# Performance work log

Hardware: AMD Instinct MI355X
Metric: run time of the kernel (lower is better)

The kernel has to match this reference:

```python
import jax, jax.numpy as jnp
import numpy as np

REG = 0.01  # cfg['mf']['reg']
NUM_USERS, NUM_ITEMS, H = 100000, 1000000, 64
B, K = 16384, 50


def setup_inputs() -> dict:
    key = jax.random.key(0)
    k1, k2, k3, k4, k5 = jax.random.split(key, 5)
    return {
        "user_weight": jax.random.normal(k1, (NUM_USERS, H), dtype=jnp.float32),
        "item_weight": jax.random.normal(k2, (NUM_ITEMS, H), dtype=jnp.float32),
        "user_bias": jnp.zeros((NUM_USERS, 1), dtype=jnp.float32),
        "item_bias": jnp.zeros((NUM_ITEMS, 1), dtype=jnp.float32),
        "bias": jnp.zeros((1,), dtype=jnp.float32),
        "target": jax.random.uniform(k3, (B, K), dtype=jnp.float32),
        "user": jax.random.randint(k4, (B,), 0, NUM_USERS),
        "item": jax.random.randint(k5, (B, K), 0, NUM_ITEMS),
    }


def reference(user_weight, item_weight, user_bias, item_bias, bias, target, user, item):
    # user_embedding(u) = user_weight[u] + user_bias[u] (scalar bias broadcast over H)
    ue = user_weight[user] + user_bias[user]            # [B, H]
    ie = item_weight[item] + item_bias[item]            # [B, K, H]
    # per-user dot against its K items + global scalar bias (replaces Python loop)
    pred = jnp.einsum('bh,bkh->bk', ue, ie) + bias[0]   # [B, K]
    mse = jnp.mean((pred - target) ** 2)
    reg = REG * jnp.mean(jnp.linalg.norm(ue, axis=-1)) \
        + REG * jnp.mean(jnp.linalg.norm(ie.reshape(-1, ie.shape[-1]), axis=-1))
    loss = mse + reg
    # pack predictions and scalar loss into one array
    return jnp.concatenate([pred.ravel(), loss[None]])
```

## Files before the change

kernel.cpp:

```cpp
#include <hip/hip_runtime.h>

constexpr int NB = 16384;
constexpr int NK = 50;
constexpr int NH = 64;
constexpr float REG = 0.01f;
constexpr int G  = 4;


__global__ __launch_bounds__(256) void mf_main(
    const float* __restrict__ user_weight,
    const float* __restrict__ item_weight,
    const float* __restrict__ user_bias,
    const float* __restrict__ item_bias,
    const float* __restrict__ gbias,
    const float* __restrict__ target,
    const int*   __restrict__ user,
    const int*   __restrict__ item,
    float* __restrict__ out,
    float* __restrict__ acc)
{
    const int tid  = threadIdx.x;
    const int wave = tid >> 6;
    const int lane = tid & 63;
    const int kcl  = (lane < NK) ? lane : (NK - 1);
    const bool active = (lane < NK);

    __shared__ __align__(16) float s_ue[4][NH];
    __shared__ float s_red[3][4];

    const float gb = gbias[0];

    int b  = (blockIdx.x * 4 + wave) * G;
    int u  = user[b];
    int it = item[b * NK + kcl];

    float mse_acc = 0.f, ien_acc = 0.f, uen_acc = 0.f;

    #pragma unroll
    for (int g = 0; g < G; ++g) {
        const float ubv = user_bias[u];
        const float ibv = item_bias[it];
        const float tgt = target[b * NK + kcl];
        const float uev = user_weight[(size_t)u * NH + lane] + ubv;

        const float4* rowp = reinterpret_cast<const float4*>(item_weight + (size_t)it * NH);
        float4 r[16];
        #pragma unroll
        for (int i = 0; i < 16; ++i) r[i] = rowp[i];

        int nu = u, nit = it;
        if (g + 1 < G) {
            nu  = user[b + 1];
            nit = item[(b + 1) * NK + kcl];
        }

        s_ue[wave][lane] = uev;
        float us = uev * uev;
        #pragma unroll
        for (int off = 32; off > 0; off >>= 1) us += __shfl_down(us, off);
        if (lane == 0) uen_acc += sqrtf(us);

        const float4* uep = reinterpret_cast<const float4*>(&s_ue[wave][0]);
        float dot = 0.f, sq = 0.f;
        #pragma unroll
        for (int i = 0; i < 16; ++i) {
            const float4 ue4 = uep[i];
            const float iex = r[i].x + ibv;
            const float iey = r[i].y + ibv;
            const float iez = r[i].z + ibv;
            const float iew = r[i].w + ibv;
            dot += iex * ue4.x + iey * ue4.y + iez * ue4.z + iew * ue4.w;
            sq  += iex * iex   + iey * iey   + iez * iez   + iew * iew;
        }
        const float pred = dot + gb;
        if (active) {
            out[b * NK + lane] = pred;
            const float d = pred - tgt;
            mse_acc += d * d;
            ien_acc += sqrtf(sq);
        }

        b += 1; u = nu; it = nit;
    }

    #pragma unroll
    for (int off = 32; off > 0; off >>= 1) {
        mse_acc += __shfl_down(mse_acc, off);
        ien_acc += __shfl_down(ien_acc, off);
    }
    if (lane == 0) {
        s_red[0][wave] = mse_acc;
        s_red[1][wave] = uen_acc;
        s_red[2][wave] = ien_acc;
    }
    __syncthreads();
    if (tid == 0) {
        atomicAdd(&acc[0], s_red[0][0] + s_red[0][1] + s_red[0][2] + s_red[0][3]);
        atomicAdd(&acc[1], s_red[1][0] + s_red[1][1] + s_red[1][2] + s_red[1][3]);
        atomicAdd(&acc[2], s_red[2][0] + s_red[2][1] + s_red[2][2] + s_red[2][3]);
    }
}

__global__ void mf_finish(const float* __restrict__ acc, float* __restrict__ out)
{
    const float inv_bk = 1.0f / (float)(NB * NK);
    const float mse = acc[0] * inv_bk;
    const float loss = mse + REG * (acc[1] / (float)NB) + REG * (acc[2] * inv_bk);
    out[NB * NK] = loss;
}

extern "C" void kernel_launch(void* const* d_in, const int* in_sizes, int n_in,
                              void* d_out, int out_size, void* d_ws, size_t ws_size,
                              hipStream_t stream) {
    const float* user_weight = (const float*)d_in[0];
    const float* item_weight = (const float*)d_in[1];
    const float* user_bias   = (const float*)d_in[2];
    const float* item_bias   = (const float*)d_in[3];
    const float* gbias       = (const float*)d_in[4];
    const float* target      = (const float*)d_in[5];
    const int*   user        = (const int*)d_in[6];
    const int*   item        = (const int*)d_in[7];
    float* out = (float*)d_out;
    float* acc = (float*)d_ws;

    hipMemsetAsync(acc, 0, 3 * sizeof(float), stream);
    mf_main<<<NB / (4 * G), 256, 0, stream>>>(user_weight, item_weight, user_bias, item_bias,
                                              gbias, target, user, item, out, acc);
    mf_finish<<<1, 1, 0, stream>>>(acc, out);
}
```

Baseline: 370.4 us.

## Gather item rows cooperatively with 16 lanes per row and shuffle reductions

Each item row was loaded by a single lane as 16 strided float4 reads. Now 16 lanes read one row together as contiguous float4 loads, so each wave fetches four rows per instruction with coalesced 256-byte accesses, and the dot products are reduced with 16-lane shuffles. The user embedding stays in registers instead of shared memory, and users per wave drop from 4 to 2. The cost is many more shuffle instructions per row and fewer users batched per wave.

Result: slower. 403.0 us (+8.8%).

```diff
diff --git a/kernel.cpp b/kernel.cpp
--- a/kernel.cpp
+++ b/kernel.cpp
@@ -4,7 +4,8 @@
 constexpr int NK = 50;
 constexpr int NH = 64;
 constexpr float REG = 0.01f;
-constexpr int G  = 4;
+constexpr int G  = 2;
+constexpr int NGRP = (NK + 3) / 4;
 
 
 __global__ __launch_bounds__(256) void mf_main(
@@ -22,72 +23,85 @@
     const int tid  = threadIdx.x;
     const int wave = tid >> 6;
     const int lane = tid & 63;
-    const int kcl  = (lane < NK) ? lane : (NK - 1);
-    const bool active = (lane < NK);
+    const int q    = lane >> 4;
+    const int l16  = lane & 15;
+    const bool lk  = (lane < NK);
+    const int lcl  = lk ? lane : 0;
 
-    __shared__ __align__(16) float s_ue[4][NH];
     __shared__ float s_red[3][4];
 
     const float gb = gbias[0];
 
-    int b  = (blockIdx.x * 4 + wave) * G;
-    int u  = user[b];
-    int it = item[b * NK + kcl];
+    int b = (blockIdx.x * 4 + wave) * G;
+
+    int   u    = user[b];
+    int   kidx = item[b * NK + lcl];
+    float tgt  = target[b * NK + lcl];
 
     float mse_acc = 0.f, ien_acc = 0.f, uen_acc = 0.f;
 
     #pragma unroll
     for (int g = 0; g < G; ++g) {
         const float ubv = user_bias[u];
-        const float ibv = item_bias[it];
-        const float tgt = target[b * NK + kcl];
-        const float uev = user_weight[(size_t)u * NH + lane] + ubv;
+        const float4 uw4 = *reinterpret_cast<const float4*>(user_weight + (size_t)u * NH + l16 * 4);
+        const float ibv = lk ? item_bias[kidx] : 0.f;
 
-        const float4* rowp = reinterpret_cast<const float4*>(item_weight + (size_t)it * NH);
-        float4 r[16];
+        float4 r[NGRP];
         #pragma unroll
-        for (int i = 0; i < 16; ++i) r[i] = rowp[i];
-
-        int nu = u, nit = it;
-        if (g + 1 < G) {
-            nu  = user[b + 1];
-            nit = item[(b + 1) * NK + kcl];
+        for (int gr = 0; gr < NGRP; ++gr) {
+            int k = gr * 4 + q;
+            int kk = (k < NK) ? k : (NK - 1);
+            const int it = __shfl(kidx, kk);
+            r[gr] = *reinterpret_cast<const float4*>(item_weight + (size_t)it * NH + l16 * 4);
         }
 
-        s_ue[wave][lane] = uev;
-        float us = uev * uev;
+        int nu = u, nkidx = kidx; float ntgt = tgt;
+        if (g + 1 < G) {
+            nu    = user[b + 1];
+            nkidx = item[(b + 1) * NK + lcl];
+            ntgt  = target[(b + 1) * NK + lcl];
+        }
+
+        const float4 ue4 = make_float4(uw4.x + ubv, uw4.y + ubv, uw4.z + ubv, uw4.w + ubv);
+        float us = ue4.x * ue4.x + ue4.y * ue4.y + ue4.z * ue4.z + ue4.w * ue4.w;
         #pragma unroll
-        for (int off = 32; off > 0; off >>= 1) us += __shfl_down(us, off);
+        for (int off = 8; off > 0; off >>= 1) us += __shfl_down(us, off, 16);
         if (lane == 0) uen_acc += sqrtf(us);
 
-        const float4* uep = reinterpret_cast<const float4*>(&s_ue[wave][0]);
-        float dot = 0.f, sq = 0.f;
         #pragma unroll
-        for (int i = 0; i < 16; ++i) {
-            const float4 ue4 = uep[i];
-            const float iex = r[i].x + ibv;
-            const float iey = r[i].y + ibv;
-            const float iez = r[i].z + ibv;
-            const float iew = r[i].w + ibv;
-            dot += iex * ue4.x + iey * ue4.y + iez * ue4.z + iew * ue4.w;
-            sq  += iex * iex   + iey * iey   + iez * iez   + iew * iew;
-        }
-        const float pred = dot + gb;
-        if (active) {
-            out[b * NK + lane] = pred;
-            const float d = pred - tgt;
-            mse_acc += d * d;
-            ien_acc += sqrtf(sq);
+        for (int gr = 0; gr < NGRP; ++gr) {
+            const int k  = gr * 4 + q;
+            const int kk = (k < NK) ? k : (NK - 1);
+            const float ib = __shfl(ibv, kk);
+            const float tg = __shfl(tgt, kk);
+            const float iex = r[gr].x + ib;
+            const float iey = r[gr].y + ib;
+            const float iez = r[gr].z + ib;
+            const float iew = r[gr].w + ib;
+            float pdot = iex * ue4.x + iey * ue4.y + iez * ue4.z + iew * ue4.w;
+            float psq  = iex * iex   + iey * iey   + iez * iez   + iew * iew;
+            #pragma unroll
+            for (int off = 8; off > 0; off >>= 1) {
+                pdot += __shfl_down(pdot, off, 16);
+                psq  += __shfl_down(psq,  off, 16);
+            }
+            if (l16 == 0 && k < NK) {
+                const float pred = pdot + gb;
+                out[b * NK + k] = pred;
+                const float d = pred - tg;
+                mse_acc += d * d;
+                ien_acc += sqrtf(psq);
+            }
         }
 
-        b += 1; u = nu; it = nit;
+        b += 1; u = nu; kidx = nkidx; tgt = ntgt;
     }
 
-    #pragma unroll
-    for (int off = 32; off > 0; off >>= 1) {
-        mse_acc += __shfl_down(mse_acc, off);
-        ien_acc += __shfl_down(ien_acc, off);
-    }
+    mse_acc += __shfl_down(mse_acc, 32);
+    mse_acc += __shfl_down(mse_acc, 16);
+    ien_acc += __shfl_down(ien_acc, 32);
+    ien_acc += __shfl_down(ien_acc, 16);
+
     if (lane == 0) {
         s_red[0][wave] = mse_acc;
         s_red[1][wave] = uen_acc;
```

## Coalesce item-row gathers via cooperative float4 loads staged through swizzled LDS

Applied to the files above, without the earlier changes.

Each wave now loads item rows cooperatively, with 16 lanes covering one 256-byte row using float4 loads. This replaces the pattern where each lane fetched its own whole row, which gave poorly coalesced gathers. Rows are written to an XOR-swizzled shared buffer so the per-lane dot products read without bank conflicts. The loads for the next user are issued before the current compute as a software prefetch. The change costs 51KB of LDS per block, more __syncthreads-free LDS traffic, and a launch_bounds occupancy hint, and all of this may limit occupancy.

Result: no change. 368.4 us (-0.5%).

```diff
diff --git a/kernel.cpp b/kernel.cpp
--- a/kernel.cpp
+++ b/kernel.cpp
@@ -5,9 +5,9 @@
 constexpr int NH = 64;
 constexpr float REG = 0.01f;
 constexpr int G  = 4;
+constexpr int NGRP = 13;
 
-
-__global__ __launch_bounds__(256) void mf_main(
+__global__ __launch_bounds__(256, 3) void mf_main(
     const float* __restrict__ user_weight,
     const float* __restrict__ item_weight,
     const float* __restrict__ user_bias,
@@ -22,65 +22,95 @@
     const int tid  = threadIdx.x;
     const int wave = tid >> 6;
     const int lane = tid & 63;
-    const int kcl  = (lane < NK) ? lane : (NK - 1);
+    const int q    = lane >> 4;
+    const int l16  = lane & 15;
     const bool active = (lane < NK);
+    const int kcl  = active ? lane : (NK - 1);
 
+    __shared__ __align__(16) float s_it[4][NK * NH];
     __shared__ __align__(16) float s_ue[4][NH];
     __shared__ float s_red[3][4];
 
+    float* __restrict__ sit = s_it[wave];
+    float* __restrict__ sue = s_ue[wave];
+
     const float gb = gbias[0];
 
-    int b  = (blockIdx.x * 4 + wave) * G;
-    int u  = user[b];
-    int it = item[b * NK + kcl];
+    int b = (blockIdx.x * 4 + wave) * G;
+
+    int   u    = user[b];
+    int   kidx = item[b * NK + kcl];
+    float ubv  = user_bias[u];
+    float tgt  = target[b * NK + kcl];
+    float ibv  = item_bias[kidx];
+    float uev  = user_weight[(size_t)u * NH + lane] + ubv;
+
+    float4 r[NGRP];
+    #pragma unroll
+    for (int gr = 0; gr < NGRP; ++gr) {
+        const int k  = gr * 4 + q;
+        const int kk = (k < NK) ? k : (NK - 1);
+        const int it = __shfl(kidx, kk);
+        r[gr] = *reinterpret_cast<const float4*>(item_weight + (size_t)it * NH + l16 * 4);
+    }
 
     float mse_acc = 0.f, ien_acc = 0.f, uen_acc = 0.f;
 
     #pragma unroll
     for (int g = 0; g < G; ++g) {
-        const float ubv = user_bias[u];
-        const float ibv = item_bias[it];
-        const float tgt = target[b * NK + kcl];
-        const float uev = user_weight[(size_t)u * NH + lane] + ubv;
+        #pragma unroll
+        for (int gr = 0; gr < NGRP; ++gr) {
+            const int k  = gr * 4 + q;
+            const int ks = (k < NK) ? k : (NK - 1);
+            *reinterpret_cast<float4*>(sit + ks * NH + ((l16 ^ (ks & 15)) << 2)) = r[gr];
+        }
+        sue[lane] = uev;
 
-        const float4* rowp = reinterpret_cast<const float4*>(item_weight + (size_t)it * NH);
-        float4 r[16];
-        #pragma unroll
-        for (int i = 0; i < 16; ++i) r[i] = rowp[i];
-
-        int nu = u, nit = it;
-        if (g + 1 < G) {
-            nu  = user[b + 1];
-            nit = item[(b + 1) * NK + kcl];
-        }
-
-        s_ue[wave][lane] = uev;
         float us = uev * uev;
         #pragma unroll
         for (int off = 32; off > 0; off >>= 1) us += __shfl_down(us, off);
         if (lane == 0) uen_acc += sqrtf(us);
 
-        const float4* uep = reinterpret_cast<const float4*>(&s_ue[wave][0]);
+        const float ibv_c = ibv, tgt_c = tgt;
+
+        if (g + 1 < G) {
+            u    = user[b + 1];
+            kidx = item[(b + 1) * NK + kcl];
+            ubv  = user_bias[u];
+            tgt  = target[(b + 1) * NK + kcl];
+            ibv  = item_bias[kidx];
+            uev  = user_weight[(size_t)u * NH + lane] + ubv;
+            #pragma unroll
+            for (int gr = 0; gr < NGRP; ++gr) {
+                const int k  = gr * 4 + q;
+                const int kk = (k < NK) ? k : (NK - 1);
+                const int it = __shfl(kidx, kk);
+                r[gr] = *reinterpret_cast<const float4*>(item_weight + (size_t)it * NH + l16 * 4);
+            }
+        }
+
+        const int ksw = kcl & 15;
+        const float* rowbase = sit + kcl * NH;
         float dot = 0.f, sq = 0.f;
         #pragma unroll
-        for (int i = 0; i < 16; ++i) {
-            const float4 ue4 = uep[i];
-            const float iex = r[i].x + ibv;
-            const float iey = r[i].y + ibv;
-            const float iez = r[i].z + ibv;
-            const float iew = r[i].w + ibv;
-            dot += iex * ue4.x + iey * ue4.y + iez * ue4.z + iew * ue4.w;
-            sq  += iex * iex   + iey * iey   + iez * iez   + iew * iew;
+        for (int j = 0; j < 16; ++j) {
+            const float4 iv = *reinterpret_cast<const float4*>(rowbase + ((j ^ ksw) << 2));
+            const float4 uv = *reinterpret_cast<const float4*>(sue + (j << 2));
+            const float iex = iv.x + ibv_c;
+            const float iey = iv.y + ibv_c;
+            const float iez = iv.z + ibv_c;
+            const float iew = iv.w + ibv_c;
+            dot += iex * uv.x + iey * uv.y + iez * uv.z + iew * uv.w;
+            sq  += iex * iex  + iey * iey  + iez * iez  + iew * iew;
         }
         const float pred = dot + gb;
         if (active) {
             out[b * NK + lane] = pred;
-            const float d = pred - tgt;
+            const float d = pred - tgt_c;
             mse_acc += d * d;
             ien_acc += sqrtf(sq);
         }
-
-        b += 1; u = nu; it = nit;
+        b += 1;
     }
 
     #pragma unroll
```
